# Performance work log

Hardware: AMD Instinct MI355X
Metric: run time of the kernel (lower is better)

The kernel has to match this reference:

```python
import jax, jax.numpy as jnp
import numpy as np

H = 16  # n_heads
D = 1024  # embed_dim == input_dim
FF = 4 * D
EPS = 1e-5  # torch LayerNorm default


def layer_norm(x, g, b):
    m = x.mean(-1, keepdims=True)
    v = x.var(-1, keepdims=True)
    return (x - m) / jnp.sqrt(v + EPS) * g + b


def setup_inputs() -> dict:
    key = jax.random.key(0)
    ks = jax.random.split(key, 8)
    s = lambda k, sh: (jax.random.normal(k, sh, jnp.float32) * 0.02)
    return {
        "kq": jax.random.normal(ks[0], (4, 2048, 512), jnp.float32),
        "v": jax.random.normal(ks[1], (4, 2048, 512), jnp.float32),
        "Wk": s(ks[2], (D, D)), "bk": jnp.zeros((D,), jnp.float32),
        "Wq": s(ks[3], (D, D)), "bq": jnp.zeros((D,), jnp.float32),
        "Wv": s(ks[4], (D, D)), "bv": jnp.zeros((D,), jnp.float32),
        "W1": s(ks[5], (FF, D)), "b1": jnp.zeros((FF,), jnp.float32),
        "W2": s(ks[6], (D, FF)), "b2": jnp.zeros((D,), jnp.float32),
        "g1": jnp.ones((D,), jnp.float32), "be1": jnp.zeros((D,), jnp.float32),
        "g2": jnp.ones((D,), jnp.float32), "be2": jnp.zeros((D,), jnp.float32),
    }


def reference(kq, v, Wk, bk, Wq, bq, Wv, bv, W1, b1, W2, b2, g1, be1, g2, be2):
    X = jnp.concatenate([kq, v], axis=-1)  # [n, T, input_dim]
    n, T, _ = kq.shape

    def heads(y):  # [n, T, D] -> [n, H, T, hd]
        return y.reshape(n, T, H, -1).transpose(0, 2, 1, 3)

    K = heads(X @ Wk.T + bk)
    Q = heads(X @ Wq.T + bq)
    V = heads(X @ Wv.T + bv)

    # NOTE: source applies no 1/sqrt(head_dim) scaling
    scores = jnp.einsum('nhqd,nhkd->nhqk', Q, K)
    causal = jnp.tril(jnp.ones((T, T), bool))  # mask = -inf strictly above diagonal
    scores = jnp.where(causal, scores, -jnp.inf)
    A = jax.nn.softmax(scores, axis=-1)
    attn_out = jnp.einsum('nhqk,nhkd->nhqd', A, V)
    attn_out = attn_out.transpose(0, 2, 1, 3).reshape(n, T, -1)  # [n, T, D]

    Vflat = V.transpose(0, 2, 1, 3).reshape(n, T, -1)  # residual is V projection, per source
    h = layer_norm(Vflat + attn_out, g1, be1)
    ff = jax.nn.gelu(h @ W1.T + b1, approximate=False) @ W2.T + b2  # torch GELU default = exact erf
    return layer_norm(h + ff, g2, be2)
```

## Files before the change

### kernel.cpp

```cpp
#include <hip/hip_runtime.h>
#include <stdint.h>

#define SEQ 2048
#define DM  1024
#define NH  16
#define HD  64
#define FFD 4096
#define TOK 8192

typedef __bf16 bf16x8 __attribute__((ext_vector_type(8)));
typedef float  f32x4  __attribute__((ext_vector_type(4)));
typedef float  f32x16 __attribute__((ext_vector_type(16)));
typedef unsigned short u16x8 __attribute__((ext_vector_type(8)));
typedef unsigned short u16x4 __attribute__((ext_vector_type(4)));
typedef unsigned int   u32x4 __attribute__((ext_vector_type(4)));

__device__ __forceinline__ unsigned short f2bf(float f) {
  unsigned u = __builtin_bit_cast(unsigned, f);
  u += 0x7fffu + ((u >> 16) & 1u);
  return (unsigned short)(u >> 16);
}
__device__ __forceinline__ float bf2f(unsigned short h) {
  return __builtin_bit_cast(float, ((unsigned)h) << 16);
}
__device__ __forceinline__ f32x4 mfma16(bf16x8 a, bf16x8 b, f32x4 c) {
  return __builtin_amdgcn_mfma_f32_16x16x32_bf16(a, b, c, 0, 0, 0);
}
__device__ __forceinline__ f32x16 mfma32(bf16x8 a, bf16x8 b, f32x16 c) {
  return __builtin_amdgcn_mfma_f32_32x32x16_bf16(a, b, c, 0, 0, 0);
}
__device__ __forceinline__ unsigned cvtpk(float lo, float hi) {
  unsigned r;
  asm("v_cvt_pk_bf16_f32 %0, %1, %2" : "=v"(r) : "v"(lo), "v"(hi));
  return r;
}
__device__ __forceinline__ void gld_lds16(void* lds, const void* g) {
  __builtin_amdgcn_global_load_lds((__attribute__((address_space(1))) void*)g,
                                   (__attribute__((address_space(3))) void*)lds,
                                   16, 0, 0);
}

__global__ __launch_bounds__(256) void concat_cast(
    const float* __restrict__ kq, const float* __restrict__ v,
    unsigned short* __restrict__ X) {
  int i = (blockIdx.x * 256 + threadIdx.x) * 4;
  int tkn = i >> 10;
  int c = i & 1023;
  const float* s = (c < 512) ? (kq + (size_t)tkn * 512 + c)
                             : (v  + (size_t)tkn * 512 + (c - 512));
  f32x4 f = *(const f32x4*)s;
  u16x4 o = { f2bf(f[0]), f2bf(f[1]), f2bf(f[2]), f2bf(f[3]) };
  *(u16x4*)&X[i] = o;
}

__global__ __launch_bounds__(256) void cast_f2b(
    const float* __restrict__ src, unsigned short* __restrict__ dst, int n) {
  int i = (blockIdx.x * 256 + threadIdx.x) * 4;
  if (i >= n) return;
  f32x4 f = *(const f32x4*)&src[i];
  u16x4 o = { f2bf(f[0]), f2bf(f[1]), f2bf(f[2]), f2bf(f[3]) };
  *(u16x4*)&dst[i] = o;
}

__global__ __launch_bounds__(256) void bias3(
    const float* __restrict__ a, const float* __restrict__ b,
    const float* __restrict__ c, float* __restrict__ o) {
  int i = blockIdx.x * 256 + threadIdx.x;
  if (i < 1024) o[i] = a[i];
  else if (i < 2048) o[i] = b[i - 1024];
  else if (i < 3072) o[i] = c[i - 2048];
}

template<int BM, int EPI>
__global__ __launch_bounds__(512, 2) void gemm256(
    const unsigned short* __restrict__ A, const unsigned short* __restrict__ B,
    const float* __restrict__ bias, void* __restrict__ Cout,
    void* __restrict__ CoutQ, void* __restrict__ CoutV, void* __restrict__ CoutVI,
    int M, int N, int K, int PR, int PC, int NPC) {
  constexpr int MF = BM / 32;
  constexpr int MG = MF / 4;
  extern __shared__ __align__(16) unsigned short lds[];
  unsigned short* Asm0 = lds;
  unsigned short* Bsm0 = lds + 2 * BM * 64;
  const int tid = threadIdx.x;
  const int w = tid >> 6, l = tid & 63, lr = l & 15, lg = l >> 4;
  const int wm = w >> 2, wn = w & 3;
  const int bid = blockIdx.x;
  const int xcd = bid & 7;
  const int i = bid >> 3;
  const int patch_r = xcd / NPC, patch_c = xcd % NPC;
  const int bm = (patch_r * PR + (i % PR)) * BM;
  const int bn = (patch_c * PC + (i / PR)) * 256;
  const int NT = K >> 6;
  const int srow = tid >> 3;
  const int sc8  = tid & 7;

  f32x4 acc[MF][4] = {};

  auto stage = [&](int kt, int bb) {
    unsigned short* da = Asm0 + bb * (BM * 64);
    unsigned short* db = Bsm0 + bb * (256 * 64);
#pragma unroll
    for (int p = 0; p < BM / 64; ++p) {
      int row = p * 64 + srow;
      gld_lds16(da + (p * 512 + w * 64) * 8,
                &A[(size_t)(bm + row) * K + kt * 64 + ((sc8 ^ (row & 7)) << 3)]);
    }
#pragma unroll
    for (int p = 0; p < 4; ++p) {
      int row = p * 64 + srow;
      gld_lds16(db + (p * 512 + w * 64) * 8,
                &B[(size_t)(bn + row) * K + kt * 64 + ((sc8 ^ (row & 7)) << 3)]);
    }
  };

  stage(0, 0);

  for (int t = 0; t < NT; ++t) {
    asm volatile("s_waitcnt vmcnt(0)" ::: "memory");
    __builtin_amdgcn_s_barrier();
    if (t + 1 < NT) stage(t + 1, (t + 1) & 1);
    const unsigned short* As = Asm0 + (t & 1) * (BM * 64);
    const unsigned short* Bs = Bsm0 + (t & 1) * (256 * 64);
    bf16x8 bv[4][2];
#pragma unroll
    for (int fn = 0; fn < 4; ++fn)
#pragma unroll
      for (int kk = 0; kk < 2; ++kk) {
        int row = wn * 64 + fn * 16 + lr;
        int c8 = (kk * 4 + lg) ^ (row & 7);
        bv[fn][kk] = *(const bf16x8*)&Bs[row * 64 + c8 * 8];
      }
#pragma unroll
    for (int mg = 0; mg < MG; ++mg) {
      bf16x8 av[4][2];
#pragma unroll
      for (int fr = 0; fr < 4; ++fr)
#pragma unroll
        for (int kk = 0; kk < 2; ++kk) {
          int row = wm * (BM / 2) + (mg * 4 + fr) * 16 + lr;
          int c8 = (kk * 4 + lg) ^ (row & 7);
          av[fr][kk] = *(const bf16x8*)&As[row * 64 + c8 * 8];
        }
      __builtin_amdgcn_s_setprio(1);
#pragma unroll
      for (int fr = 0; fr < 4; ++fr)
#pragma unroll
        for (int fn = 0; fn < 4; ++fn)
#pragma unroll
          for (int kk = 0; kk < 2; ++kk)
            acc[mg * 4 + fr][fn] = mfma16(av[fr][kk], bv[fn][kk], acc[mg * 4 + fr][fn]);
      __builtin_amdgcn_s_setprio(0);
    }
  }
#pragma unroll
  for (int mf = 0; mf < MF; ++mf) {
    int row0 = bm + wm * (BM / 2) + mf * 16 + lg * 4;
#pragma unroll
    for (int nf = 0; nf < 4; ++nf) {
      int col = bn + wn * 64 + nf * 16 + lr;
      float bcol = bias[col];
#pragma unroll
      for (int r = 0; r < 4; ++r) {
        float vv = acc[mf][nf][r] + bcol;
        int row = row0 + r;
        if (EPI == 2) vv = 0.5f * vv * (1.0f + erff(vv * 0.70710678118654752f));
        if (EPI == 0) {
          ((float*)Cout)[(size_t)row * N + col] = vv;
        } else if (EPI == 5) {
          int third = col >> 10, c = col & 1023;
          unsigned short hv = f2bf(vv);
          int bb = row >> 11, tt = row & 2047;
          if (third == 0) {
            int hh = c >> 6, dc = (c >> 4) & 3, dl = c & 15;
            ((unsigned short*)Cout)[((((size_t)(bb * 16 + hh) * 4 + dc) * 2048 + tt) << 4) + dl] = hv;
          } else if (third == 1) {
            ((unsigned short*)CoutQ)[(size_t)row * 1024 + c] = hv;
          } else {
            ((unsigned short*)CoutV)[(size_t)row * 1024 + c] = hv;
            int hh = c >> 6, d = c & 63;
            ((unsigned short*)CoutVI)[((((size_t)(bb * 16 + hh) * 128 + (tt >> 4)) * 64 + d) << 4) + (tt & 15)] = hv;
          }
        } else {
          ((unsigned short*)Cout)[(size_t)row * N + col] = f2bf(vv);
        }
      }
    }
  }
}

__global__ __launch_bounds__(128, 4) void attn_kernel(
    const unsigned short* __restrict__ Q, const unsigned short* __restrict__ KI,
    const unsigned short* __restrict__ VI, unsigned short* __restrict__ O) {
  __shared__ __align__(16) unsigned short T[2][32 * 72];
  const int tid = threadIdx.x;
  const int w = tid >> 6, l = tid & 63;
  const int q32 = l & 31;
  const int g = l >> 5;
  const int x = blockIdx.x;
  const int bh = (x & 7) * 8 + (x >> 3);
  const int b = bh >> 4, h = bh & 15;
  const int u = 63 - (2 * (int)blockIdx.y + w);
  const size_t tok0 = (size_t)b * SEQ;
  const size_t hoff = (size_t)h * 64;
  const unsigned short* Kp = KI + (size_t)bh * 4 * SEQ * 16;
  const unsigned short* Vp = VI + (size_t)bh * 128 * 64 * 16;

  const int q0 = u * 32;
  const int qg = q0 + q32;

  bf16x8 qf[4];
#pragma unroll
  for (int ks = 0; ks < 4; ++ks)
    qf[ks] = *(const bf16x8*)&Q[(tok0 + qg) * DM + hoff + ks * 16 + g * 8];

  f32x16 ot0 = {}, ot1 = {};
  float m = -3.0e38f, lden = 0.f;

  bf16x8 kf[4], vf[4];
#pragma unroll
  for (int ks = 0; ks < 4; ++ks)
    kf[ks] = *(const bf16x8*)&Kp[((size_t)ks * SEQ + q32) * 16 + g * 8];
#pragma unroll
  for (int dt = 0; dt < 2; ++dt)
#pragma unroll
    for (int s = 0; s < 2; ++s)
      vf[dt * 2 + s] = *(const bf16x8*)&Vp[((size_t)s * 64 + dt * 32 + q32) * 16 + g * 8];

#pragma unroll 1
  for (int j = 0; j <= u; ++j) {
    f32x16 st = {};
    __builtin_amdgcn_s_setprio(1);
#pragma unroll
    for (int ks = 0; ks < 4; ++ks) st = mfma32(kf[ks], qf[ks], st);
    __builtin_amdgcn_s_setprio(0);
    const int jn = (j < u) ? j + 1 : u;
    bf16x8 kn[4], vn[4];
#pragma unroll
    for (int ks = 0; ks < 4; ++ks)
      kn[ks] = *(const bf16x8*)&Kp[((size_t)ks * SEQ + jn * 32 + q32) * 16 + g * 8];
#pragma unroll
    for (int dt = 0; dt < 2; ++dt)
#pragma unroll
      for (int s = 0; s < 2; ++s)
        vn[dt * 2 + s] = *(const bf16x8*)&Vp[(((size_t)jn * 2 + s) * 64 + dt * 32 + q32) * 16 + g * 8];
    if (j == u) {
#pragma unroll
      for (int r = 0; r < 16; ++r) {
        int kg = j * 32 + (r & 3) + 8 * (r >> 2) + 4 * g;
        if (kg > qg) st[r] = -3.0e38f;
      }
    }
    float x0 = fmaxf(st[0], st[1]),  x1 = fmaxf(st[2], st[3]);
    float x2 = fmaxf(st[4], st[5]),  x3 = fmaxf(st[6], st[7]);
    float x4 = fmaxf(st[8], st[9]),  x5 = fmaxf(st[10], st[11]);
    float x6 = fmaxf(st[12], st[13]), x7 = fmaxf(st[14], st[15]);
    x0 = fmaxf(x0, x1); x2 = fmaxf(x2, x3); x4 = fmaxf(x4, x5); x6 = fmaxf(x6, x7);
    x0 = fmaxf(x0, x2); x4 = fmaxf(x4, x6);
    float pmax = fmaxf(x0, x4);
    if (__any(pmax - m > 8.0f)) {
      float pp = fmaxf(pmax, __shfl_xor(pmax, 32, 64));
      float mnew = fmaxf(m, pp);
      float sc = __expf(m - mnew);
#pragma unroll
      for (int r = 0; r < 16; ++r) { ot0[r] *= sc; ot1[r] *= sc; }
      lden *= sc;
      m = mnew;
    }
    float p[16];
#pragma unroll
    for (int r = 0; r < 16; ++r) p[r] = __expf(st[r] - m);
    {
      float s0 = p[0] + p[1], s1 = p[2] + p[3], s2 = p[4] + p[5], s3 = p[6] + p[7];
      float s4 = p[8] + p[9], s5 = p[10] + p[11], s6 = p[12] + p[13], s7 = p[14] + p[15];
      s0 += s1; s2 += s3; s4 += s5; s6 += s7;
      s0 += s2; s4 += s6;
      lden += s0 + s4;
    }
    unsigned c0 = cvtpk(p[0], p[1]),   c1 = cvtpk(p[2], p[3]);
    unsigned c2 = cvtpk(p[4], p[5]),   c3 = cvtpk(p[6], p[7]);
    unsigned c4 = cvtpk(p[8], p[9]),   c5 = cvtpk(p[10], p[11]);
    unsigned c6 = cvtpk(p[12], p[13]), c7 = cvtpk(p[14], p[15]);
    unsigned y0 = __shfl_xor(c0, 32, 64), y1 = __shfl_xor(c1, 32, 64);
    unsigned y2 = __shfl_xor(c2, 32, 64), y3 = __shfl_xor(c3, 32, 64);
    unsigned y4 = __shfl_xor(c4, 32, 64), y5 = __shfl_xor(c5, 32, 64);
    unsigned y6 = __shfl_xor(c6, 32, 64), y7 = __shfl_xor(c7, 32, 64);
    u32x4 f0 = { g ? y2 : c0, g ? y3 : c1, g ? c2 : y0, g ? c3 : y1 };
    u32x4 f1 = { g ? y6 : c4, g ? y7 : c5, g ? c6 : y4, g ? c7 : y5 };
    bf16x8 pb0 = __builtin_bit_cast(bf16x8, f0);
    bf16x8 pb1 = __builtin_bit_cast(bf16x8, f1);
    __builtin_amdgcn_s_setprio(1);
    ot0 = mfma32(vf[0], pb0, ot0);
    ot0 = mfma32(vf[1], pb1, ot0);
    ot1 = mfma32(vf[2], pb0, ot1);
    ot1 = mfma32(vf[3], pb1, ot1);
    __builtin_amdgcn_s_setprio(0);
#pragma unroll
    for (int ks = 0; ks < 4; ++ks) kf[ks] = kn[ks];
#pragma unroll
    for (int q = 0; q < 4; ++q) vf[q] = vn[q];
  }
  lden += __shfl_xor(lden, 32, 64);
  float inv = 1.0f / lden;
#pragma unroll
  for (int r = 0; r < 16; ++r) {
    int d = (r & 3) + 8 * (r >> 2) + 4 * g;
    T[w][q32 * 72 + d]      = f2bf(ot0[r] * inv);
    T[w][q32 * 72 + 32 + d] = f2bf(ot1[r] * inv);
  }
#pragma unroll
  for (int j2 = 0; j2 < 4; ++j2) {
    int col = g * 32 + j2 * 8;
    u16x8 vv = *(const u16x8*)&T[w][q32 * 72 + col];
    *(u16x8*)&O[(tok0 + q0 + q32) * DM + hoff + col] = vv;
  }
}

template<int MODE>
__global__ __launch_bounds__(256) void ln_kernel(
    const unsigned short* __restrict__ Xa, const void* __restrict__ Xc,
    const float* __restrict__ g, const float* __restrict__ be,
    void* __restrict__ outp) {
  const int row = blockIdx.x, t = threadIdx.x;
  const size_t base = (size_t)row * DM + t * 4;
  float x[4];
  u16x4 a = *(const u16x4*)&Xa[base];
  if (MODE == 0) {
    u16x4 c = *(const u16x4*)&((const unsigned short*)Xc)[base];
#pragma unroll
    for (int i = 0; i < 4; ++i) x[i] = bf2f(a[i]) + bf2f(c[i]);
  } else {
    f32x4 c = *(const f32x4*)&((const float*)Xc)[base];
#pragma unroll
    for (int i = 0; i < 4; ++i) x[i] = bf2f(a[i]) + c[i];
  }
  float s = x[0] + x[1] + x[2] + x[3];
  float ss = x[0] * x[0] + x[1] * x[1] + x[2] * x[2] + x[3] * x[3];
#pragma unroll
  for (int m = 1; m < 64; m <<= 1) {
    s  += __shfl_xor(s, m, 64);
    ss += __shfl_xor(ss, m, 64);
  }
  __shared__ float red[8];
  const int w = t >> 6;
  if ((t & 63) == 0) { red[w * 2] = s; red[w * 2 + 1] = ss; }
  __syncthreads();
  s  = red[0] + red[2] + red[4] + red[6];
  ss = red[1] + red[3] + red[5] + red[7];
  const float mean = s * (1.0f / DM);
  const float var = ss * (1.0f / DM) - mean * mean;
  const float rstd = rsqrtf(var + 1e-5f);
  if (MODE == 0) {
    u16x4 o;
#pragma unroll
    for (int i = 0; i < 4; ++i) {
      int cx = t * 4 + i;
      o[i] = f2bf((x[i] - mean) * rstd * g[cx] + be[cx]);
    }
    *(u16x4*)&((unsigned short*)outp)[base] = o;
  } else {
    f32x4 o;
#pragma unroll
    for (int i = 0; i < 4; ++i) {
      int cx = t * 4 + i;
      o[i] = (x[i] - mean) * rstd * g[cx] + be[cx];
    }
    *(f32x4*)&((float*)outp)[base] = o;
  }
}

extern "C" void kernel_launch(void* const* d_in, const int* in_sizes, int n_in,
                              void* d_out, int out_size, void* d_ws, size_t ws_size,
                              hipStream_t stream) {
  (void)in_sizes; (void)n_in; (void)out_size; (void)ws_size;
  const float* kq  = (const float*)d_in[0];
  const float* v   = (const float*)d_in[1];
  const float* Wk  = (const float*)d_in[2];
  const float* bk  = (const float*)d_in[3];
  const float* Wq  = (const float*)d_in[4];
  const float* bq  = (const float*)d_in[5];
  const float* Wv  = (const float*)d_in[6];
  const float* bv  = (const float*)d_in[7];
  const float* W1  = (const float*)d_in[8];
  const float* b1  = (const float*)d_in[9];
  const float* W2  = (const float*)d_in[10];
  const float* b2  = (const float*)d_in[11];
  const float* g1  = (const float*)d_in[12];
  const float* be1 = (const float*)d_in[13];
  const float* g2  = (const float*)d_in[14];
  const float* be2 = (const float*)d_in[15];
  float* out = (float*)d_out;
  uint8_t* ws = (uint8_t*)d_ws;

  unsigned short* Xb   = (unsigned short*)(ws + 0);
  unsigned short* Wkb  = (unsigned short*)(ws + 16777216);
  unsigned short* Wqb  = (unsigned short*)(ws + 18874368);
  unsigned short* Wvb  = (unsigned short*)(ws + 20971520);
  unsigned short* Qb   = (unsigned short*)(ws + 23068672);
  unsigned short* Kb   = (unsigned short*)(ws + 39845888);
  unsigned short* Ab   = (unsigned short*)(ws + 56623104);
  unsigned short* F1b  = (unsigned short*)(ws + 0);
  unsigned short* W1b  = (unsigned short*)(ws + 73400320);
  unsigned short* W2b  = (unsigned short*)(ws + 81788928);
  unsigned short* Vb   = (unsigned short*)(ws + 90177536);
  unsigned short* Hb   = (unsigned short*)(ws + 106954752);
  float*          F2f  = (float*)(ws + 123731968);
  unsigned short* VIg  = (unsigned short*)(ws + 123731968);
  float*          bqkv = (float*)(ws + 140509184);

  concat_cast<<<TOK * DM / 1024, 256, 0, stream>>>(kq, v, Xb);
  cast_f2b<<<1024, 256, 0, stream>>>(Wk, Wkb, DM * DM);
  cast_f2b<<<1024, 256, 0, stream>>>(Wq, Wqb, DM * DM);
  cast_f2b<<<1024, 256, 0, stream>>>(Wv, Wvb, DM * DM);
  cast_f2b<<<4096, 256, 0, stream>>>(W1, W1b, FFD * DM);
  cast_f2b<<<4096, 256, 0, stream>>>(W2, W2b, DM * FFD);
  bias3<<<12, 256, 0, stream>>>(bk, bq, bv, bqkv);

  gemm256<128, 5><<<768, 512, 98304, stream>>>(
      Xb, Wkb, bqkv, Kb, Qb, Vb, VIg, TOK, 3072, DM, 8, 12, 1);

  attn_kernel<<<dim3(64, 32), 128, 0, stream>>>(Qb, Kb, VIg, Ab);

  ln_kernel<0><<<TOK, 256, 0, stream>>>(Vb, Ab, g1, be1, Hb);

  gemm256<256, 2><<<512, 512, 131072, stream>>>(
      Hb, W1b, b1, F1b, nullptr, nullptr, nullptr, TOK, FFD, DM, 8, 8, 2);
  gemm256<128, 0><<<256, 512, 98304, stream>>>(
      F1b, W2b, b2, F2f, nullptr, nullptr, nullptr, TOK, DM, FFD, 8, 4, 1);

  ln_kernel<1><<<TOK, 256, 0, stream>>>(Hb, F2f, g2, be2, out);
}
```

Baseline: 376.0 us.

## Replace templated GEMM with fixed 128x256 tile, K-step 32, higher occupancy

```diff
diff --git a/kernel.cpp b/kernel.cpp
--- a/kernel.cpp
+++ b/kernel.cpp
@@ -71,17 +71,15 @@
   else if (i < 3072) o[i] = c[i - 2048];
 }
 
-template<int BM, int EPI>
-__global__ __launch_bounds__(512, 2) void gemm256(
+template<int EPI>
+__global__ __launch_bounds__(512, 4) void gemm128(
     const unsigned short* __restrict__ A, const unsigned short* __restrict__ B,
     const float* __restrict__ bias, void* __restrict__ Cout,
     void* __restrict__ CoutQ, void* __restrict__ CoutV, void* __restrict__ CoutVI,
-    int M, int N, int K, int PR, int PC, int NPC) {
-  constexpr int MF = BM / 32;
-  constexpr int MG = MF / 4;
+    int M, int N, int LDK, int NT, int PR, int PC, int NPC) {
   extern __shared__ __align__(16) unsigned short lds[];
   unsigned short* Asm0 = lds;
-  unsigned short* Bsm0 = lds + 2 * BM * 64;
+  unsigned short* Bsm0 = lds + 2 * 128 * 32;
   const int tid = threadIdx.x;
   const int w = tid >> 6, l = tid & 63, lr = l & 15, lg = l >> 4;
   const int wm = w >> 2, wn = w & 3;
@@ -89,28 +87,22 @@
   const int xcd = bid & 7;
   const int i = bid >> 3;
   const int patch_r = xcd / NPC, patch_c = xcd % NPC;
-  const int bm = (patch_r * PR + (i % PR)) * BM;
+  const int bm = (patch_r * PR + (i % PR)) * 128;
   const int bn = (patch_c * PC + (i / PR)) * 256;
-  const int NT = K >> 6;
-  const int srow = tid >> 3;
-  const int sc8  = tid & 7;
-
-  f32x4 acc[MF][4] = {};
-
+
+  f32x4 acc[4][4] = {};
+
+  const int sr = tid >> 2, ss = tid & 3;
   auto stage = [&](int kt, int bb) {
-    unsigned short* da = Asm0 + bb * (BM * 64);
-    unsigned short* db = Bsm0 + bb * (256 * 64);
-#pragma unroll
-    for (int p = 0; p < BM / 64; ++p) {
-      int row = p * 64 + srow;
-      gld_lds16(da + (p * 512 + w * 64) * 8,
-                &A[(size_t)(bm + row) * K + kt * 64 + ((sc8 ^ (row & 7)) << 3)]);
-    }
-#pragma unroll
-    for (int p = 0; p < 4; ++p) {
-      int row = p * 64 + srow;
-      gld_lds16(db + (p * 512 + w * 64) * 8,
-                &B[(size_t)(bn + row) * K + kt * 64 + ((sc8 ^ (row & 7)) << 3)]);
+    unsigned short* da = Asm0 + bb * (128 * 32);
+    unsigned short* db = Bsm0 + bb * (256 * 32);
+    gld_lds16(da + tid * 8,
+              &A[(size_t)(bm + sr) * LDK + kt * 32 + ((ss ^ ((sr >> 1) & 3)) << 3)]);
+#pragma unroll
+    for (int p = 0; p < 2; ++p) {
+      int rb = p * 128 + sr;
+      gld_lds16(db + (p * 512 + tid) * 8,
+                &B[(size_t)(bn + rb) * LDK + kt * 32 + ((ss ^ ((rb >> 1) & 3)) << 3)]);
     }
   };
 
@@ -120,42 +112,32 @@
     asm volatile("s_waitcnt vmcnt(0)" ::: "memory");
     __builtin_amdgcn_s_barrier();
     if (t + 1 < NT) stage(t + 1, (t + 1) & 1);
-    const unsigned short* As = Asm0 + (t & 1) * (BM * 64);
-    const unsigned short* Bs = Bsm0 + (t & 1) * (256 * 64);
-    bf16x8 bv[4][2];
-#pragma unroll
-    for (int fn = 0; fn < 4; ++fn)
-#pragma unroll
-      for (int kk = 0; kk < 2; ++kk) {
-        int row = wn * 64 + fn * 16 + lr;
-        int c8 = (kk * 4 + lg) ^ (row & 7);
-        bv[fn][kk] = *(const bf16x8*)&Bs[row * 64 + c8 * 8];
-      }
-#pragma unroll
-    for (int mg = 0; mg < MG; ++mg) {
-      bf16x8 av[4][2];
-#pragma unroll
-      for (int fr = 0; fr < 4; ++fr)
-#pragma unroll
-        for (int kk = 0; kk < 2; ++kk) {
-          int row = wm * (BM / 2) + (mg * 4 + fr) * 16 + lr;
-          int c8 = (kk * 4 + lg) ^ (row & 7);
-          av[fr][kk] = *(const bf16x8*)&As[row * 64 + c8 * 8];
-        }
-      __builtin_amdgcn_s_setprio(1);
-#pragma unroll
-      for (int fr = 0; fr < 4; ++fr)
-#pragma unroll
-        for (int fn = 0; fn < 4; ++fn)
-#pragma unroll
-          for (int kk = 0; kk < 2; ++kk)
-            acc[mg * 4 + fr][fn] = mfma16(av[fr][kk], bv[fn][kk], acc[mg * 4 + fr][fn]);
-      __builtin_amdgcn_s_setprio(0);
-    }
-  }
-#pragma unroll
-  for (int mf = 0; mf < MF; ++mf) {
-    int row0 = bm + wm * (BM / 2) + mf * 16 + lg * 4;
+    const unsigned short* As = Asm0 + (t & 1) * (128 * 32);
+    const unsigned short* Bs = Bsm0 + (t & 1) * (256 * 32);
+    bf16x8 av[4], bv[4];
+#pragma unroll
+    for (int nf = 0; nf < 4; ++nf) {
+      int row = wn * 64 + nf * 16 + lr;
+      int sl = lg ^ ((row >> 1) & 3);
+      bv[nf] = *(const bf16x8*)&Bs[row * 32 + sl * 8];
+    }
+#pragma unroll
+    for (int fr = 0; fr < 4; ++fr) {
+      int row = wm * 64 + fr * 16 + lr;
+      int sl = lg ^ ((row >> 1) & 3);
+      av[fr] = *(const bf16x8*)&As[row * 32 + sl * 8];
+    }
+    __builtin_amdgcn_s_setprio(1);
+#pragma unroll
+    for (int fr = 0; fr < 4; ++fr)
+#pragma unroll
+      for (int nf = 0; nf < 4; ++nf)
+        acc[fr][nf] = mfma16(av[fr], bv[nf], acc[fr][nf]);
+    __builtin_amdgcn_s_setprio(0);
+  }
+#pragma unroll
+  for (int mf = 0; mf < 4; ++mf) {
+    int row0 = bm + wm * 64 + mf * 16 + lg * 4;
 #pragma unroll
     for (int nf = 0; nf < 4; ++nf) {
       int col = bn + wn * 64 + nf * 16 + lr;
@@ -416,17 +398,17 @@
   cast_f2b<<<4096, 256, 0, stream>>>(W2, W2b, DM * FFD);
   bias3<<<12, 256, 0, stream>>>(bk, bq, bv, bqkv);
 
-  gemm256<128, 5><<<768, 512, 98304, stream>>>(
-      Xb, Wkb, bqkv, Kb, Qb, Vb, VIg, TOK, 3072, DM, 8, 12, 1);
+  gemm128<5><<<768, 512, 49152, stream>>>(
+      Xb, Wkb, bqkv, Kb, Qb, Vb, VIg, TOK, 3072, DM, 32, 8, 12, 1);
 
   attn_kernel<<<dim3(64, 32), 128, 0, stream>>>(Qb, Kb, VIg, Ab);
 
   ln_kernel<0><<<TOK, 256, 0, stream>>>(Vb, Ab, g1, be1, Hb);
 
-  gemm256<256, 2><<<512, 512, 131072, stream>>>(
-      Hb, W1b, b1, F1b, nullptr, nullptr, nullptr, TOK, FFD, DM, 8, 8, 2);
-  gemm256<128, 0><<<256, 512, 98304, stream>>>(
-      F1b, W2b, b2, F2f, nullptr, nullptr, nullptr, TOK, DM, FFD, 8, 4, 1);
+  gemm128<2><<<1024, 512, 49152, stream>>>(
+      Hb, W1b, b1, F1b, nullptr, nullptr, nullptr, TOK, FFD, DM, 32, 16, 8, 2);
+  gemm128<0><<<256, 512, 49152, stream>>>(
+      F1b, W2b, b2, F2f, nullptr, nullptr, nullptr, TOK, DM, FFD, 128, 8, 4, 1);
 
   ln_kernel<1><<<TOK, 256, 0, stream>>>(Hb, F2f, g2, be2, out);
 }
```

Result: slower. 388.0 us (+3.2%).

## Triple-buffer GEMM LDS staging with partial vmcnt waits and fixed 128-row tiles

Applied to the files above, without the earlier changes.

```diff
diff --git a/kernel.cpp b/kernel.cpp
--- a/kernel.cpp
+++ b/kernel.cpp
@@ -71,17 +71,15 @@
   else if (i < 3072) o[i] = c[i - 2048];
 }
 
-template<int BM, int EPI>
-__global__ __launch_bounds__(512, 2) void gemm256(
+template<int EPI>
+__global__ __launch_bounds__(512, 2) void gemm3(
     const unsigned short* __restrict__ A, const unsigned short* __restrict__ B,
     const float* __restrict__ bias, void* __restrict__ Cout,
     void* __restrict__ CoutQ, void* __restrict__ CoutV, void* __restrict__ CoutVI,
     int M, int N, int K, int PR, int PC, int NPC) {
-  constexpr int MF = BM / 32;
-  constexpr int MG = MF / 4;
   extern __shared__ __align__(16) unsigned short lds[];
   unsigned short* Asm0 = lds;
-  unsigned short* Bsm0 = lds + 2 * BM * 64;
+  unsigned short* Bsm0 = lds + 3 * 128 * 64;
   const int tid = threadIdx.x;
   const int w = tid >> 6, l = tid & 63, lr = l & 15, lg = l >> 4;
   const int wm = w >> 2, wn = w & 3;
@@ -89,19 +87,19 @@
   const int xcd = bid & 7;
   const int i = bid >> 3;
   const int patch_r = xcd / NPC, patch_c = xcd % NPC;
-  const int bm = (patch_r * PR + (i % PR)) * BM;
+  const int bm = (patch_r * PR + (i % PR)) * 128;
   const int bn = (patch_c * PC + (i / PR)) * 256;
   const int NT = K >> 6;
   const int srow = tid >> 3;
   const int sc8  = tid & 7;
 
-  f32x4 acc[MF][4] = {};
+  f32x4 acc[4][4] = {};
 
   auto stage = [&](int kt, int bb) {
-    unsigned short* da = Asm0 + bb * (BM * 64);
+    unsigned short* da = Asm0 + bb * (128 * 64);
     unsigned short* db = Bsm0 + bb * (256 * 64);
 #pragma unroll
-    for (int p = 0; p < BM / 64; ++p) {
+    for (int p = 0; p < 2; ++p) {
       int row = p * 64 + srow;
       gld_lds16(da + (p * 512 + w * 64) * 8,
                 &A[(size_t)(bm + row) * K + kt * 64 + ((sc8 ^ (row & 7)) << 3)]);
@@ -115,14 +113,16 @@
   };
 
   stage(0, 0);
+  stage(1, 1);
 
   for (int t = 0; t < NT; ++t) {
-    asm volatile("s_waitcnt vmcnt(0)" ::: "memory");
+    if (t + 1 < NT) asm volatile("s_waitcnt vmcnt(6)" ::: "memory");
+    else            asm volatile("s_waitcnt vmcnt(0)" ::: "memory");
     __builtin_amdgcn_s_barrier();
-    if (t + 1 < NT) stage(t + 1, (t + 1) & 1);
-    const unsigned short* As = Asm0 + (t & 1) * (BM * 64);
-    const unsigned short* Bs = Bsm0 + (t & 1) * (256 * 64);
-    bf16x8 bv[4][2];
+    if (t + 2 < NT) stage(t + 2, (t + 2) % 3);
+    const unsigned short* As = Asm0 + (t % 3) * (128 * 64);
+    const unsigned short* Bs = Bsm0 + (t % 3) * (256 * 64);
+    bf16x8 av[4][2], bv[4][2];
 #pragma unroll
     for (int fn = 0; fn < 4; ++fn)
 #pragma unroll
@@ -132,30 +132,26 @@
         bv[fn][kk] = *(const bf16x8*)&Bs[row * 64 + c8 * 8];
       }
 #pragma unroll
-    for (int mg = 0; mg < MG; ++mg) {
-      bf16x8 av[4][2];
-#pragma unroll
-      for (int fr = 0; fr < 4; ++fr)
-#pragma unroll
-        for (int kk = 0; kk < 2; ++kk) {
-          int row = wm * (BM / 2) + (mg * 4 + fr) * 16 + lr;
-          int c8 = (kk * 4 + lg) ^ (row & 7);
-          av[fr][kk] = *(const bf16x8*)&As[row * 64 + c8 * 8];
-        }
-      __builtin_amdgcn_s_setprio(1);
-#pragma unroll
-      for (int fr = 0; fr < 4; ++fr)
-#pragma unroll
-        for (int fn = 0; fn < 4; ++fn)
-#pragma unroll
-          for (int kk = 0; kk < 2; ++kk)
-            acc[mg * 4 + fr][fn] = mfma16(av[fr][kk], bv[fn][kk], acc[mg * 4 + fr][fn]);
-      __builtin_amdgcn_s_setprio(0);
-    }
-  }
-#pragma unroll
-  for (int mf = 0; mf < MF; ++mf) {
-    int row0 = bm + wm * (BM / 2) + mf * 16 + lg * 4;
+    for (int fr = 0; fr < 4; ++fr)
+#pragma unroll
+      for (int kk = 0; kk < 2; ++kk) {
+        int row = wm * 64 + fr * 16 + lr;
+        int c8 = (kk * 4 + lg) ^ (row & 7);
+        av[fr][kk] = *(const bf16x8*)&As[row * 64 + c8 * 8];
+      }
+    __builtin_amdgcn_s_setprio(1);
+#pragma unroll
+    for (int fr = 0; fr < 4; ++fr)
+#pragma unroll
+      for (int nf = 0; nf < 4; ++nf)
+#pragma unroll
+        for (int kk = 0; kk < 2; ++kk)
+          acc[fr][nf] = mfma16(av[fr][kk], bv[nf][kk], acc[fr][nf]);
+    __builtin_amdgcn_s_setprio(0);
+  }
+#pragma unroll
+  for (int mf = 0; mf < 4; ++mf) {
+    int row0 = bm + wm * 64 + mf * 16 + lg * 4;
 #pragma unroll
     for (int nf = 0; nf < 4; ++nf) {
       int col = bn + wn * 64 + nf * 16 + lr;
@@ -416,16 +412,16 @@
   cast_f2b<<<4096, 256, 0, stream>>>(W2, W2b, DM * FFD);
   bias3<<<12, 256, 0, stream>>>(bk, bq, bv, bqkv);
 
-  gemm256<128, 5><<<768, 512, 98304, stream>>>(
+  gemm3<5><<<768, 512, 147456, stream>>>(
       Xb, Wkb, bqkv, Kb, Qb, Vb, VIg, TOK, 3072, DM, 8, 12, 1);
 
   attn_kernel<<<dim3(64, 32), 128, 0, stream>>>(Qb, Kb, VIg, Ab);
 
   ln_kernel<0><<<TOK, 256, 0, stream>>>(Vb, Ab, g1, be1, Hb);
 
-  gemm256<256, 2><<<512, 512, 131072, stream>>>(
-      Hb, W1b, b1, F1b, nullptr, nullptr, nullptr, TOK, FFD, DM, 8, 8, 2);
-  gemm256<128, 0><<<256, 512, 98304, stream>>>(
+  gemm3<2><<<1024, 512, 147456, stream>>>(
+      Hb, W1b, b1, F1b, nullptr, nullptr, nullptr, TOK, FFD, DM, 8, 16, 1);
+  gemm3<0><<<256, 512, 147456, stream>>>(
       F1b, W2b, b2, F2f, nullptr, nullptr, nullptr, TOK, DM, FFD, 8, 4, 1);
 
   ln_kernel<1><<<TOK, 256, 0, stream>>>(Hb, F2f, g2, be2, out);
```

After: 396.1 us. +5.4%, slower.
